# Kernel tuning notes

Hardware: AMD Instinct MI355X
Metric: run time of the kernel (lower is better)

## Reference

```python
import jax, jax.numpy as jnp
import numpy as np

KEEP_RATIO = 0.5  # init kwarg keep_ratio
B, S, D = 8, 8192, 1024


def setup_inputs() -> dict:
    key = jax.random.key(0)
    k1, k2, k3 = jax.random.split(key, 3)
    hidden_states = jax.random.normal(k1, (B, S, D), dtype=jnp.float32)
    active_mask = jax.random.bernoulli(k2, 0.8, (B, S))
    scorer_w = jax.random.normal(k3, (D,), dtype=jnp.float32) / np.sqrt(D)
    scorer_b = jnp.zeros((1,), dtype=jnp.float32)
    return {"hidden_states": hidden_states, "active_mask": active_mask,
            "scorer_w": scorer_w, "scorer_b": scorer_b}


def reference(hidden_states, active_mask, scorer_w, scorer_b):
    # scores = Linear(d_model -> 1).squeeze(-1)  -> [B, S]
    scores = jnp.einsum('bsd,d->bs', hidden_states, scorer_w) + scorer_b[0]
    # masked_fill(~active, -inf)
    masked = jnp.where(active_mask, scores, -jnp.inf)
    # per-row variable k = max(1, ceil(n_active * keep_ratio))
    n_active = jnp.sum(active_mask, axis=-1)                      # [B] int
    k = jnp.maximum(1, jnp.ceil(n_active.astype(jnp.float32) * KEEP_RATIO)).astype(jnp.int32)
    # rank of each token within its row by descending masked score;
    # inactive tokens (-inf) sort last, so rank < k selects the top-k active tokens
    order = jnp.argsort(-masked, axis=-1)      # [B, S] indices, best first
    ranks = jnp.argsort(order, axis=-1)        # [B, S] rank per position
    keep_mask = (ranks < k[:, None]) & active_mask
    return keep_mask
```

## Files before the change

kernel.cpp:

```cpp
#include <hip/hip_runtime.h>
#include <math.h>

#define BB 8
#define SS 8192
#define DD 1024

__global__ __launch_bounds__(256) void score_kernel(
    const float* __restrict__ hs, const int* __restrict__ mask,
    const float* __restrict__ w, const float* __restrict__ bias,
    float* __restrict__ scores)
{
    const int wid = threadIdx.x >> 6;
    const int lane = threadIdx.x & 63;
    const int token = blockIdx.x * 4 + wid;

    const float4* hp = (const float4*)(hs + (size_t)token * DD);
    const float4* wp = (const float4*)w;

    float sum = 0.f;
#pragma unroll
    for (int j = 0; j < 4; ++j) {
        float4 h = hp[lane + j * 64];
        float4 ww = wp[lane + j * 64];
        sum += h.x * ww.x + h.y * ww.y + h.z * ww.z + h.w * ww.w;
    }
#pragma unroll
    for (int off = 32; off > 0; off >>= 1)
        sum += __shfl_down(sum, off, 64);

    if (lane == 0) {
        bool act = mask[token] != 0;
        scores[token] = act ? (sum + bias[0]) : -INFINITY;
    }
}

__global__ __launch_bounds__(1024) void select_kernel(
    const int* __restrict__ mask, float* __restrict__ buf)
{
    __shared__ unsigned int keys[SS];
    __shared__ unsigned int hist[256];
    __shared__ unsigned int sbuf[256];
    __shared__ unsigned int wsum[16];
    __shared__ unsigned int n_active_sh;
    __shared__ unsigned int sel_bin, sel_knew;

    const int row = blockIdx.x;
    const int tid = threadIdx.x;
    const float* srow = buf + row * SS;
    const int* mrow = mask + row * SS;

    if (tid == 0) n_active_sh = 0;
    __syncthreads();

    unsigned int mycnt = 0;
    for (int i = tid; i < SS; i += 1024) {
        unsigned int u = __float_as_uint(srow[i]);
        keys[i] = (u & 0x80000000u) ? ~u : (u | 0x80000000u);
        if (mrow[i] != 0) mycnt++;
    }
    atomicAdd(&n_active_sh, mycnt);
    __syncthreads();

    const unsigned int n_active = n_active_sh;
    unsigned int k = (n_active + 1u) >> 1;
    if (k < 1u) k = 1u;

    unsigned int prefix = 0, prefmask = 0;
    for (int round = 0; round < 4; ++round) {
        const int shift = 24 - 8 * round;
        if (tid < 256) hist[tid] = 0;
        __syncthreads();
        for (int i = tid; i < SS; i += 1024) {
            unsigned int key = keys[i];
            if ((key & prefmask) == prefix)
                atomicAdd(&hist[(key >> shift) & 0xFFu], 1u);
        }
        __syncthreads();
        if (tid < 256) sbuf[tid] = hist[tid];
        __syncthreads();
        for (int off = 1; off < 256; off <<= 1) {
            unsigned int v = 0;
            if (tid < 256 && tid + off < 256) v = sbuf[tid + off];
            __syncthreads();
            if (tid < 256) sbuf[tid] += v;
            __syncthreads();
        }
        if (tid < 256) {
            unsigned int above = (tid < 255) ? sbuf[tid + 1] : 0u;
            if (sbuf[tid] >= k && above < k) {
                sel_bin = (unsigned int)tid;
                sel_knew = k - above;
            }
        }
        __syncthreads();
        prefix |= sel_bin << shift;
        prefmask |= 0xFFu << shift;
        k = sel_knew;
        __syncthreads();
    }

    const unsigned int thr = prefix;
    const unsigned int k_rem = k;

    const int base = tid * 8;
    unsigned int cnt = 0;
#pragma unroll
    for (int j = 0; j < 8; ++j) cnt += (keys[base + j] == thr) ? 1u : 0u;

    const int lane = tid & 63, wv = tid >> 6;
    unsigned int inc = cnt;
#pragma unroll
    for (int off = 1; off < 64; off <<= 1) {
        unsigned int n = (unsigned int)__shfl_up((int)inc, off, 64);
        if (lane >= off) inc += n;
    }
    if (lane == 63) wsum[wv] = inc;
    __syncthreads();
    if (tid == 0) {
        unsigned int acc = 0;
        for (int i = 0; i < 16; ++i) { unsigned int t = wsum[i]; wsum[i] = acc; acc += t; }
    }
    __syncthreads();
    unsigned int r = wsum[wv] + inc - cnt;

    int* orow = (int*)(buf + row * SS);
#pragma unroll
    for (int j = 0; j < 8; ++j) {
        const int i = base + j;
        const unsigned int key = keys[i];
        bool keep;
        if (key > thr) keep = true;
        else if (key == thr) { keep = (r < k_rem); r++; }
        else keep = false;
        keep = keep && (mrow[i] != 0);
        orow[i] = keep ? 1 : 0;
    }
}

extern "C" void kernel_launch(void* const* d_in, const int* in_sizes, int n_in,
                              void* d_out, int out_size, void* d_ws, size_t ws_size,
                              hipStream_t stream) {
    const float* hs  = (const float*)d_in[0];
    const int* msk   = (const int*)d_in[1];
    const float* w   = (const float*)d_in[2];
    const float* bias= (const float*)d_in[3];

    float* buf = (float*)d_out;

    score_kernel<<<(BB * SS) / 4, 256, 0, stream>>>(hs, msk, w, bias, buf);
    select_kernel<<<BB, 1024, 0, stream>>>(msk, buf);
}
```

Before: 372.8 us.

## Process multiple tokens per wave in scorer and use wave-level suffix scan in select

The score kernel now launches a fixed 8192 waves, each handling eight tokens in pairs. The weight vector and bias are loaded into registers once per wave, and two rows' loads are kept in flight to raise memory-level parallelism. The select kernel replaces its 256-thread shared-memory scan, which needed about 16 barriers per round, with a single-wave shuffle-based suffix scan over 4 bins per lane. The risk is fewer resident waves, which may reduce latency hiding for the bandwidth-bound 256MB read.

```diff
diff --git a/kernel.cpp b/kernel.cpp
--- a/kernel.cpp
+++ b/kernel.cpp
@@ -4,33 +4,53 @@
 #define BB 8
 #define SS 8192
 #define DD 1024
+#define NTOK (BB * SS)
+#define NWAVES 8192
+#define TOK_PER_WAVE (NTOK / NWAVES)
+
+__device__ __forceinline__ float dot4(float4 a, float4 b) {
+    return a.x * b.x + a.y * b.y + a.z * b.z + a.w * b.w;
+}
 
 __global__ __launch_bounds__(256) void score_kernel(
     const float* __restrict__ hs, const int* __restrict__ mask,
     const float* __restrict__ w, const float* __restrict__ bias,
     float* __restrict__ scores)
 {
-    const int wid = threadIdx.x >> 6;
+    const int gw   = blockIdx.x * 4 + (threadIdx.x >> 6);
     const int lane = threadIdx.x & 63;
-    const int token = blockIdx.x * 4 + wid;
 
-    const float4* hp = (const float4*)(hs + (size_t)token * DD);
     const float4* wp = (const float4*)w;
+    const float4 w0 = wp[lane];
+    const float4 w1 = wp[lane + 64];
+    const float4 w2 = wp[lane + 128];
+    const float4 w3 = wp[lane + 192];
+    const float b = bias[0];
 
-    float sum = 0.f;
 #pragma unroll
-    for (int j = 0; j < 4; ++j) {
-        float4 h = hp[lane + j * 64];
-        float4 ww = wp[lane + j * 64];
-        sum += h.x * ww.x + h.y * ww.y + h.z * ww.z + h.w * ww.w;
-    }
+    for (int t = 0; t < TOK_PER_WAVE; t += 2) {
+        const int tokA = t * NWAVES + gw;
+        const int tokB = (t + 1) * NWAVES + gw;
+        const float4* hA = (const float4*)(hs + (size_t)tokA * DD);
+        const float4* hB = (const float4*)(hs + (size_t)tokB * DD);
+
+        float4 a0 = hA[lane];       float4 a1 = hA[lane + 64];
+        float4 a2 = hA[lane + 128]; float4 a3 = hA[lane + 192];
+        float4 c0 = hB[lane];       float4 c1 = hB[lane + 64];
+        float4 c2 = hB[lane + 128]; float4 c3 = hB[lane + 192];
+
+        float sA = dot4(a0, w0) + dot4(a1, w1) + dot4(a2, w2) + dot4(a3, w3);
+        float sB = dot4(c0, w0) + dot4(c1, w1) + dot4(c2, w2) + dot4(c3, w3);
+
 #pragma unroll
-    for (int off = 32; off > 0; off >>= 1)
-        sum += __shfl_down(sum, off, 64);
-
-    if (lane == 0) {
-        bool act = mask[token] != 0;
-        scores[token] = act ? (sum + bias[0]) : -INFINITY;
+        for (int off = 32; off > 0; off >>= 1) {
+            sA += __shfl_down(sA, off, 64);
+            sB += __shfl_down(sB, off, 64);
+        }
+        if (lane == 0) {
+            scores[tokA] = (mask[tokA] != 0) ? (sA + b) : -INFINITY;
+            scores[tokB] = (mask[tokB] != 0) ? (sB + b) : -INFINITY;
+        }
     }
 }
 
@@ -39,7 +59,6 @@
 {
     __shared__ unsigned int keys[SS];
     __shared__ unsigned int hist[256];
-    __shared__ unsigned int sbuf[256];
     __shared__ unsigned int wsum[16];
     __shared__ unsigned int n_active_sh;
     __shared__ unsigned int sel_bin, sel_knew;
@@ -76,21 +95,28 @@
                 atomicAdd(&hist[(key >> shift) & 0xFFu], 1u);
         }
         __syncthreads();
-        if (tid < 256) sbuf[tid] = hist[tid];
-        __syncthreads();
-        for (int off = 1; off < 256; off <<= 1) {
-            unsigned int v = 0;
-            if (tid < 256 && tid + off < 256) v = sbuf[tid + off];
-            __syncthreads();
-            if (tid < 256) sbuf[tid] += v;
-            __syncthreads();
-        }
-        if (tid < 256) {
-            unsigned int above = (tid < 255) ? sbuf[tid + 1] : 0u;
-            if (sbuf[tid] >= k && above < k) {
-                sel_bin = (unsigned int)tid;
-                sel_knew = k - above;
+        if (tid < 64) {
+            const int lane = tid;
+            unsigned int h0 = hist[4 * lane];
+            unsigned int h1 = hist[4 * lane + 1];
+            unsigned int h2 = hist[4 * lane + 2];
+            unsigned int h3 = hist[4 * lane + 3];
+            unsigned int local = h0 + h1 + h2 + h3;
+            unsigned int suf = local;
+#pragma unroll
+            for (int off = 1; off < 64; off <<= 1) {
+                unsigned int v = (unsigned int)__shfl_down((int)suf, off, 64);
+                if (lane + off < 64) suf += v;
             }
+            unsigned int above = suf - local;
+            unsigned int s3 = h3 + above;
+            unsigned int s2 = h2 + s3;
+            unsigned int s1 = h1 + s2;
+            unsigned int s0 = h0 + s1;
+            if (s3 >= k && above < k) { sel_bin = 4u*lane + 3u; sel_knew = k - above; }
+            if (s2 >= k && s3    < k) { sel_bin = 4u*lane + 2u; sel_knew = k - s3; }
+            if (s1 >= k && s2    < k) { sel_bin = 4u*lane + 1u; sel_knew = k - s2; }
+            if (s0 >= k && s1    < k) { sel_bin = 4u*lane;      sel_knew = k - s1; }
         }
         __syncthreads();
         prefix |= sel_bin << shift;
@@ -140,13 +166,13 @@
 extern "C" void kernel_launch(void* const* d_in, const int* in_sizes, int n_in,
                               void* d_out, int out_size, void* d_ws, size_t ws_size,
                               hipStream_t stream) {
-    const float* hs  = (const float*)d_in[0];
-    const int* msk   = (const int*)d_in[1];
-    const float* w   = (const float*)d_in[2];
-    const float* bias= (const float*)d_in[3];
+    const float* hs   = (const float*)d_in[0];
+    const int* msk    = (const int*)d_in[1];
+    const float* w    = (const float*)d_in[2];
+    const float* bias = (const float*)d_in[3];
 
     float* buf = (float*)d_out;
 
-    score_kernel<<<(BB * SS) / 4, 256, 0, stream>>>(hs, msk, w, bias, buf);
+    score_kernel<<<NWAVES / 4, 256, 0, stream>>>(hs, msk, w, bias, buf);
     select_kernel<<<BB, 1024, 0, stream>>>(msk, buf);
 }
```

New measurement: 374.3 us. About the same (+0.4%).
